# Optimization experiments

Hardware: AMD Instinct MI355X
Metric: run time of the kernel (lower is better)

Reference implementation:

```python
import jax, jax.numpy as jnp
from jax import lax
import numpy as np

D_MODEL = 1024
D_STATE = 16
D_CONV = 4
EXPAND = 2
D_INNER = EXPAND * D_MODEL
DT_RANK = -(-D_MODEL // D_STATE)  # ceil(d_model/d_state) = 64
BATCH, SEQ = 2, 2048


def setup_inputs() -> dict:
    key = jax.random.key(0)
    ks = jax.random.split(key, 12)
    s = lambda fan_in: 1.0 / np.sqrt(fan_in)
    inp = {
        "x": jax.random.normal(ks[0], (BATCH, SEQ, D_MODEL), jnp.float32),
        # weights stored as [in, out] (i.e. torch W.T) for y = x @ W + b
        "in_proj_w": jax.random.normal(ks[1], (D_MODEL, 2 * D_INNER), jnp.float32) * s(D_MODEL),
        "in_proj_b": jax.random.normal(ks[2], (2 * D_INNER,), jnp.float32) * s(D_MODEL),
        # depthwise conv weight in torch Conv1d layout [out_ch, in_ch/groups=1, k]
        "conv_w": jax.random.normal(ks[3], (D_INNER, 1, D_CONV), jnp.float32) * s(D_CONV),
        "conv_b": jax.random.normal(ks[4], (D_INNER,), jnp.float32) * s(D_CONV),
        "x_proj_w": jax.random.normal(ks[5], (D_INNER, DT_RANK + 2 * D_STATE), jnp.float32) * s(D_INNER),
        "dt_proj_w": jax.random.normal(ks[6], (DT_RANK, D_INNER), jnp.float32) * s(DT_RANK),
        "dt_proj_b": jax.random.normal(ks[7], (D_INNER,), jnp.float32) * s(DT_RANK),
        # log_A = log(arange(1, d_state+1)) repeated over d_inner rows
        "log_A": jnp.log(jnp.broadcast_to(jnp.arange(1, D_STATE + 1, dtype=jnp.float32), (D_INNER, D_STATE))),
        "D": jnp.ones((D_INNER,), jnp.float32),
        "out_proj_w": jax.random.normal(ks[8], (D_INNER, D_MODEL), jnp.float32) * s(D_INNER),
        "out_proj_b": jax.random.normal(ks[9], (D_MODEL,), jnp.float32) * s(D_INNER),
    }
    return inp


def reference(x, in_proj_w, in_proj_b, conv_w, conv_b, x_proj_w,
              dt_proj_w, dt_proj_b, log_A, D, out_proj_w, out_proj_b):
    batch, seq_len, _ = x.shape
    d_inner, d_state = log_A.shape
    d_conv = conv_w.shape[-1]
    dt_rank = dt_proj_w.shape[0]

    xr = x @ in_proj_w + in_proj_b                      # [B, L, 2*d_inner]
    x_val, res = jnp.split(xr, 2, axis=-1)

    # depthwise causal conv: torch pads both sides by d_conv-1 then keeps first L
    # outputs, which equals left-padding by d_conv-1.
    xv = x_val.transpose(0, 2, 1)                       # [B, C, L]
    xv = lax.conv_general_dilated(xv, conv_w, window_strides=(1,),
                                  padding=[(d_conv - 1, 0)],
                                  feature_group_count=d_inner)
    xv = xv + conv_b[None, :, None]
    x_val = jax.nn.silu(xv.transpose(0, 2, 1))          # [B, L, d_inner]

    x_dbl = x_val @ x_proj_w                            # [B, L, dt_rank + 2*d_state]
    dt = x_dbl[..., :dt_rank]
    Bm = x_dbl[..., dt_rank:dt_rank + d_state]          # [B, L, N]
    Cm = x_dbl[..., dt_rank + d_state:]                 # [B, L, N]
    dt = jax.nn.softplus(dt @ dt_proj_w + dt_proj_b)    # [B, L, d_inner]

    A = -jnp.exp(log_A)                                 # [d_inner, N]

    def step(h, inputs):
        dt_t, B_t, C_t, x_t = inputs                    # [B,d], [B,N], [B,N], [B,d]
        dA = jnp.exp(dt_t[:, :, None] * A)              # [B, d_inner, N]
        h = dA * h + (dt_t * x_t)[:, :, None] * B_t[:, None, :]
        y_t = jnp.einsum('bdn,bn->bd', h, C_t)
        return h, y_t

    h0 = jnp.zeros((batch, d_inner, d_state), x.dtype)
    xs = (dt.transpose(1, 0, 2), Bm.transpose(1, 0, 2),
          Cm.transpose(1, 0, 2), x_val.transpose(1, 0, 2))
    _, ys = lax.scan(step, h0, xs)                      # ys: [L, B, d_inner]

    y = ys.transpose(1, 0, 2) + x_val * D
    return (y * jax.nn.silu(res)) @ out_proj_w + out_proj_b
```

## Files before the change

### kernel.cpp

```cpp
#include <hip/hip_runtime.h>
#include <hip/hip_bf16.h>

#define BATCH 2
#define SEQ 2048
#define DM 1024
#define DI 2048
#define DS 16
#define DR 64
#define XPC 96
#define ROWS 4096
#define NC 32
#define CL 64
#define XRLD 4096
#define KSXP 8

typedef __attribute__((ext_vector_type(8))) short bf16x8;
typedef __attribute__((ext_vector_type(4))) float f32x4;
typedef unsigned short ushort_t;
typedef unsigned int u32;

#define GLD_LDS16(g, l) \
    __builtin_amdgcn_global_load_lds((const __attribute__((address_space(1))) u32*)(g), \
                                     (__attribute__((address_space(3))) u32*)(l), 16, 0, 0)

static __device__ __forceinline__ float bf2f(ushort_t u) {
    __hip_bfloat16 b = *(__hip_bfloat16*)&u;
    return __bfloat162float(b);
}
static __device__ __forceinline__ ushort_t f2bf(float f) {
    __hip_bfloat16 b = __float2bfloat16(f);
    return *(ushort_t*)&b;
}

__global__ __launch_bounds__(256) void cvt_f32_bf16(
    const float* __restrict__ in, ushort_t* __restrict__ out)
{
    const size_t i = (size_t)(blockIdx.x * 256 + threadIdx.x) * 4;
    float4 v = *(const float4*)(in + i);
    ushort4 o;
    o.x = f2bf(v.x); o.y = f2bf(v.y); o.z = f2bf(v.z); o.w = f2bf(v.w);
    *(ushort4*)(out + i) = o;
}

__global__ __launch_bounds__(256) void convt_bf16(
    const float* __restrict__ W, ushort_t* __restrict__ Wt, int K, int N)
{
    __shared__ float t[32][33];
    const int n0 = blockIdx.x * 32, k0 = blockIdx.y * 32;
    const int tx = threadIdx.x & 31, ty = threadIdx.x >> 5;
#pragma unroll
    for (int i = 0; i < 32; i += 8)
        t[ty + i][tx] = W[(size_t)(k0 + ty + i) * N + n0 + tx];
    __syncthreads();
#pragma unroll
    for (int i = 0; i < 32; i += 8)
        Wt[(size_t)(n0 + ty + i) * K + k0 + tx] = f2bf(t[tx][ty + i]);
}

template<int EPI, typename OutT>
__global__ __launch_bounds__(256) void gemm128_bt(
    const ushort_t* __restrict__ A, const ushort_t* __restrict__ Bt,
    const float* __restrict__ bias, OutT* __restrict__ C,
    int K, int ldc)
{
    __shared__ ushort_t As[2][128 * 32];
    __shared__ ushort_t Bs[2][128 * 32];
    const int tid = threadIdx.x;
    const int lane = tid & 63, wid = tid >> 6;
    const int quad = lane >> 4, l16 = lane & 15;
    const int wr = wid >> 1, wc = wid & 1;
    const int bm = blockIdx.y, bn = blockIdx.x;

    const int sr = tid >> 2, sk = (tid & 3) << 3;
    const ushort_t* Ag0 = A + (size_t)(bm * 128 + sr) * K + sk;
    const ushort_t* Ag1 = A + (size_t)(bm * 128 + 64 + sr) * K + sk;
    const ushort_t* Bg0 = Bt + (size_t)(bn * 128 + sr) * K + sk;
    const ushort_t* Bg1 = Bt + (size_t)(bn * 128 + 64 + sr) * K + sk;

    f32x4 acc[4][4];
#pragma unroll
    for (int m = 0; m < 4; ++m)
#pragma unroll
        for (int n = 0; n < 4; ++n) acc[m][n] = (f32x4){0.f, 0.f, 0.f, 0.f};

    auto stage = [&](int buf, int kk) {
        GLD_LDS16(Ag0 + kk, &As[buf][tid * 8]);
        GLD_LDS16(Ag1 + kk, &As[buf][(tid + 256) * 8]);
        GLD_LDS16(Bg0 + kk, &Bs[buf][tid * 8]);
        GLD_LDS16(Bg1 + kk, &Bs[buf][(tid + 256) * 8]);
    };
    auto compute = [&](int buf) {
        bf16x8 a[4], b[4];
#pragma unroll
        for (int m = 0; m < 4; ++m)
            a[m] = *(const bf16x8*)&As[buf][(wr * 64 + m * 16 + l16) * 32 + 8 * quad];
#pragma unroll
        for (int n = 0; n < 4; ++n)
            b[n] = *(const bf16x8*)&Bs[buf][(wc * 64 + n * 16 + l16) * 32 + 8 * quad];
#pragma unroll
        for (int m = 0; m < 4; ++m)
#pragma unroll
            for (int n = 0; n < 4; ++n)
                acc[m][n] = __builtin_amdgcn_mfma_f32_16x16x32_bf16(
                    a[m], b[n], acc[m][n], 0, 0, 0);
    };

    const int nt = K >> 5;
    stage(0, 0);
    for (int t = 0; t < nt; t += 2) {
        __syncthreads();
        if (t + 1 < nt) stage(1, (t + 1) << 5);
        compute(0);
        __syncthreads();
        if (t + 2 < nt) stage(0, (t + 2) << 5);
        compute(1);
    }

#pragma unroll
    for (int m = 0; m < 4; ++m) {
        const int row0 = bm * 128 + wr * 64 + m * 16 + quad * 4;
#pragma unroll
        for (int n = 0; n < 4; ++n) {
            const int col = bn * 128 + wc * 64 + n * 16 + l16;
            const float bv = bias ? bias[col] : 0.f;
#pragma unroll
            for (int r = 0; r < 4; ++r) {
                float v = acc[m][n][r] + bv;
                if constexpr (EPI == 1) {
                    ((ushort_t*)C)[(size_t)(row0 + r) * ldc + col] = f2bf(v);
                } else if constexpr (EPI == 2) {
                    float sp = (v > 20.f) ? v : log1pf(__expf(v));
                    ((float*)C)[(size_t)(row0 + r) * ldc + col] = sp;
                } else {
                    ((float*)C)[(size_t)(row0 + r) * ldc + col] = v;
                }
            }
        }
    }
}

__global__ __launch_bounds__(256) void xproj_splitk(
    const ushort_t* __restrict__ A, const ushort_t* __restrict__ Bt,
    float* __restrict__ part, int K)
{
    const int BM = 64, BN = XPC;
    __shared__ ushort_t As[64 * 40];
    __shared__ ushort_t Bs[XPC * 40];
    const int tid = threadIdx.x;
    const int wid = tid >> 6, lane = tid & 63;
    const int quad = lane >> 4, l16 = lane & 15;
    const int wr = wid;
    const int bm = blockIdx.y;
    const int ks = blockIdx.x;
    const int kslc = K / KSXP;
    const int kbeg = ks * kslc;

    f32x4 acc[6];
#pragma unroll
    for (int n = 0; n < 6; ++n) acc[n] = (f32x4){0.f, 0.f, 0.f, 0.f};

    for (int k0 = kbeg; k0 < kbeg + kslc; k0 += 32) {
        for (int i = tid; i < BM * 4; i += 256) {
            int r = i >> 2, kk = (i & 3) << 3;
            *(uint4*)&As[r * 40 + kk] =
                *(const uint4*)&A[(size_t)(bm * BM + r) * K + k0 + kk];
        }
        for (int i = tid; i < BN * 4; i += 256) {
            int r = i >> 2, kk = (i & 3) << 3;
            *(uint4*)&Bs[r * 40 + kk] =
                *(const uint4*)&Bt[(size_t)r * K + k0 + kk];
        }
        __syncthreads();
        bf16x8 a, b[6];
        a = *(const bf16x8*)&As[(wr * 16 + l16) * 40 + 8 * quad];
#pragma unroll
        for (int n = 0; n < 6; ++n)
            b[n] = *(const bf16x8*)&Bs[(n * 16 + l16) * 40 + 8 * quad];
#pragma unroll
        for (int n = 0; n < 6; ++n)
            acc[n] = __builtin_amdgcn_mfma_f32_16x16x32_bf16(a, b[n], acc[n], 0, 0, 0);
        __syncthreads();
    }

    float* out = part + (size_t)ks * ROWS * XPC;
    const int row0 = bm * BM + wr * 16 + quad * 4;
#pragma unroll
    for (int n = 0; n < 6; ++n) {
        const int col = n * 16 + l16;
#pragma unroll
        for (int r = 0; r < 4; ++r)
            out[(size_t)(row0 + r) * XPC + col] = acc[n][r];
    }
}

__global__ __launch_bounds__(256) void xproj_reduce(
    const float* __restrict__ part, float* __restrict__ xdbl,
    ushort_t* __restrict__ xdt)
{
    const size_t i = (size_t)(blockIdx.x * 256 + threadIdx.x) * 4;
    float4 s = *(const float4*)(part + i);
#pragma unroll
    for (int ks = 1; ks < KSXP; ++ks) {
        float4 v = *(const float4*)(part + (size_t)ks * ROWS * XPC + i);
        s.x += v.x; s.y += v.y; s.z += v.z; s.w += v.w;
    }
    *(float4*)(xdbl + i) = s;
    const int col = (int)(i % XPC);
    if (col < DR) {
        const int row = (int)(i / XPC);
        ushort4 o;
        o.x = f2bf(s.x); o.y = f2bf(s.y); o.z = f2bf(s.z); o.w = f2bf(s.w);
        *(ushort4*)(xdt + (size_t)row * DR + col) = o;
    }
}

__global__ __launch_bounds__(256) void conv_silu_kernel(
    const ushort_t* __restrict__ xr, const float* __restrict__ cw,
    const float* __restrict__ cb, ushort_t* __restrict__ xc)
{
    int idx = blockIdx.x * 256 + threadIdx.x;
    int r = idx >> 11;
    int d = idx & (DI - 1);
    int t = r & (SEQ - 1);
    float acc = cb[d];
#pragma unroll
    for (int k = 0; k < 4; ++k) {
        int tt = t - 3 + k;
        if (tt >= 0)
            acc += bf2f(xr[(size_t)(r - 3 + k) * XRLD + d]) * cw[d * 4 + k];
    }
    float sv = acc / (1.f + __expf(-acc));
    xc[idx] = f2bf(sv);
}


__global__ __launch_bounds__(256) void scan_pass1(
    const float* __restrict__ dt, const ushort_t* __restrict__ xc,
    const float* __restrict__ xdbl, const float* __restrict__ logA,
    float* __restrict__ hend, float* __restrict__ prodA)
{
    __shared__ float Bsm[CL][DS];
    const int bid = blockIdx.x;
    const int bc = bid >> 3;
    const int d = ((bid & 7) << 8) + threadIdx.x;
    const int c = bc & (NC - 1);
    const int b = bc >> 5;
    const int r0 = b * SEQ + c * CL;

    {
        int i = threadIdx.x;
        int r = i >> 2, n4 = (i & 3) << 2;
        *(float4*)&Bsm[r][n4] = *(const float4*)&xdbl[(size_t)(r0 + r) * XPC + DR + n4];
    }
    __syncthreads();

    float A[DS], h[DS];
#pragma unroll
    for (int n = 0; n < DS; ++n) {
        A[n] = -__expf(logA[d * DS + n]);
        h[n] = 0.f;
    }
    float dtsum = 0.f;
#pragma unroll 4
    for (int t = 0; t < CL; ++t) {
        const int r = r0 + t;
        float dtv = dt[(size_t)r * DI + d];
        float xv = bf2f(xc[(size_t)r * DI + d]);
        float bx = dtv * xv;
        dtsum += dtv;
#pragma unroll
        for (int n = 0; n < DS; ++n) {
            float dA = __expf(dtv * A[n]);
            h[n] = dA * h[n] + bx * Bsm[t][n];
        }
    }
#pragma unroll
    for (int n = 0; n < DS; ++n) {
        size_t o = ((size_t)bc * DS + n) * DI + d;
        hend[o] = h[n];
        prodA[o] = __expf(dtsum * A[n]);
    }
}

__global__ __launch_bounds__(256) void scan_pass2(
    const float* __restrict__ hend, const float* __restrict__ prodA,
    float* __restrict__ hin)
{
    const int gid = blockIdx.x * 256 + threadIdx.x;
    const int d = gid & (DI - 1);
    const int bn = gid >> 11;
    const int n = bn & (DS - 1);
    const int b = bn >> 4;
    float hprev = 0.f;
#pragma unroll 8
    for (int c = 0; c < NC; ++c) {
        size_t o = ((size_t)(b * NC + c) * DS + n) * DI + d;
        hin[o] = hprev;
        hprev = prodA[o] * hprev + hend[o];
    }
}

__global__ __launch_bounds__(256) void scan_pass3(
    const float* __restrict__ dt, const ushort_t* __restrict__ xc,
    const float* __restrict__ xdbl, const ushort_t* __restrict__ res,
    const float* __restrict__ logA, const float* __restrict__ Dp,
    const float* __restrict__ hin, ushort_t* __restrict__ yg)
{
    __shared__ float BCs[CL][2 * DS];
    const int bid = blockIdx.x;
    const int bc = bid >> 3;
    const int d = ((bid & 7) << 8) + threadIdx.x;
    const int c = bc & (NC - 1);
    const int b = bc >> 5;
    const int r0 = b * SEQ + c * CL;

    {
        int i = threadIdx.x;
        int r = i >> 3, c4 = (i & 7) << 2;
        *(float4*)&BCs[r][c4] = *(const float4*)&xdbl[(size_t)(r0 + r) * XPC + DR + c4];
        int i2 = i + 256;
        int r2 = i2 >> 3, c42 = (i2 & 7) << 2;
        *(float4*)&BCs[r2][c42] = *(const float4*)&xdbl[(size_t)(r0 + r2) * XPC + DR + c42];
    }
    __syncthreads();

    float A[DS], h[DS];
#pragma unroll
    for (int n = 0; n < DS; ++n) {
        A[n] = -__expf(logA[d * DS + n]);
        h[n] = hin[((size_t)bc * DS + n) * DI + d];
    }
    const float Dd = Dp[d];
#pragma unroll 4
    for (int t = 0; t < CL; ++t) {
        const int r = r0 + t;
        float dtv = dt[(size_t)r * DI + d];
        float xv = bf2f(xc[(size_t)r * DI + d]);
        float bx = dtv * xv;
        float y = 0.f;
#pragma unroll
        for (int n = 0; n < DS; ++n) {
            float dA = __expf(dtv * A[n]);
            h[n] = dA * h[n] + bx * BCs[t][n];
            y += h[n] * BCs[t][DS + n];
        }
        y += xv * Dd;
        float rv = bf2f(res[(size_t)r * XRLD + d]);
        float sr = rv / (1.f + __expf(-rv));
        yg[(size_t)r * DI + d] = f2bf(y * sr);
    }
}

extern "C" void kernel_launch(void* const* d_in, const int* in_sizes, int n_in,
                              void* d_out, int out_size, void* d_ws, size_t ws_size,
                              hipStream_t stream) {
    const float* x          = (const float*)d_in[0];
    const float* in_proj_w  = (const float*)d_in[1];
    const float* in_proj_b  = (const float*)d_in[2];
    const float* conv_w     = (const float*)d_in[3];
    const float* conv_b     = (const float*)d_in[4];
    const float* x_proj_w   = (const float*)d_in[5];
    const float* dt_proj_w  = (const float*)d_in[6];
    const float* dt_proj_b  = (const float*)d_in[7];
    const float* log_A      = (const float*)d_in[8];
    const float* Dp         = (const float*)d_in[9];
    const float* out_proj_w = (const float*)d_in[10];
    const float* out_proj_b = (const float*)d_in[11];

    float* ws    = (float*)d_ws;
    float* dt    = ws;
    float* part  = ws;
    float* xdbl  = dt    + (size_t)ROWS * DI;
    float* hend  = xdbl  + (size_t)ROWS * XPC;
    float* prodA = hend  + (size_t)BATCH * NC * DS * DI;
    float* hin   = prodA + (size_t)BATCH * NC * DS * DI;
    ushort_t* xr     = (ushort_t*)(hin + (size_t)BATCH * NC * DS * DI);
    ushort_t* xc_bf  = xr     + (size_t)ROWS * XRLD;
    ushort_t* yg_bf  = xc_bf  + (size_t)ROWS * DI;
    ushort_t* x_bf   = yg_bf  + (size_t)ROWS * DI;
    ushort_t* wt_in  = x_bf   + (size_t)ROWS * DM;
    ushort_t* wt_out = wt_in  + (size_t)2 * DI * DM;
    ushort_t* wt_xp  = wt_out + (size_t)DM * DI;
    ushort_t* wt_dt  = wt_xp  + (size_t)XPC * DI;
    ushort_t* xdt_bf = wt_dt  + (size_t)DI * DR;

    dim3 blk(256);

    cvt_f32_bf16<<<(ROWS * DM / 4) / 256, blk, 0, stream>>>(x, x_bf);
    convt_bf16<<<dim3(2 * DI / 32, DM / 32), blk, 0, stream>>>(in_proj_w, wt_in, DM, 2 * DI);
    convt_bf16<<<dim3(DM / 32, DI / 32), blk, 0, stream>>>(out_proj_w, wt_out, DI, DM);
    convt_bf16<<<dim3(XPC / 32, DI / 32), blk, 0, stream>>>(x_proj_w, wt_xp, DI, XPC);
    convt_bf16<<<dim3(DI / 32, DR / 32), blk, 0, stream>>>(dt_proj_w, wt_dt, DR, DI);

    gemm128_bt<1, ushort_t><<<dim3(XRLD / 128, ROWS / 128), blk, 0, stream>>>(
        x_bf, wt_in, in_proj_b, xr, DM, XRLD);

    conv_silu_kernel<<<(ROWS * DI) / 256, blk, 0, stream>>>(xr, conv_w, conv_b, xc_bf);

    xproj_splitk<<<dim3(KSXP, ROWS / 64), blk, 0, stream>>>(xc_bf, wt_xp, part, DI);
    xproj_reduce<<<(ROWS * XPC / 4) / 256, blk, 0, stream>>>(part, xdbl, xdt_bf);

    gemm128_bt<2, float><<<dim3(DI / 128, ROWS / 128), blk, 0, stream>>>(
        xdt_bf, wt_dt, dt_proj_b, dt, DR, DI);

    scan_pass1<<<BATCH * NC * (DI / 256), blk, 0, stream>>>(
        dt, xc_bf, xdbl, log_A, hend, prodA);
    scan_pass2<<<(BATCH * DS * DI) / 256, blk, 0, stream>>>(hend, prodA, hin);
    scan_pass3<<<BATCH * NC * (DI / 256), blk, 0, stream>>>(
        dt, xc_bf, xdbl, xr + DI, log_A, Dp, hin, yg_bf);

    gemm128_bt<0, float><<<dim3(DM / 128, ROWS / 128), blk, 0, stream>>>(
        yg_bf, wt_out, out_proj_b, (float*)d_out, DI, DM);
}
```

Measured before the change: 287.3 us.

## Merge weight transposes, vectorize conv, store dt in bf16, split-K out_proj

Folds the four weight-transpose launches into one kernel that dispatches on block index. The depthwise conv now handles four channels per thread with vector loads. The softplus dt output is stored as bf16 to halve dt traffic in both scan passes. The out-projection GEMM is split along K into two partial sums that a separate kernel adds together with the bias, which doubles the grid from 256 to 512 blocks at the cost of extra partial-sum traffic and reduced dt precision.

After: 277.5 us. 1.04x faster.

```diff
diff --git a/kernel.cpp b/kernel.cpp
--- a/kernel.cpp
+++ b/kernel.cpp
@@ -42,11 +42,20 @@
     *(ushort4*)(out + i) = o;
 }
 
-__global__ __launch_bounds__(256) void convt_bf16(
-    const float* __restrict__ W, ushort_t* __restrict__ Wt, int K, int N)
+__global__ __launch_bounds__(256) void convt_multi(
+    const float* __restrict__ ipw, ushort_t* __restrict__ wt_in,
+    const float* __restrict__ opw, ushort_t* __restrict__ wt_out,
+    const float* __restrict__ xpw, ushort_t* __restrict__ wt_xp,
+    const float* __restrict__ dpw, ushort_t* __restrict__ wt_dt)
 {
     __shared__ float t[32][33];
-    const int n0 = blockIdx.x * 32, k0 = blockIdx.y * 32;
+    int b = blockIdx.x;
+    const float* W; ushort_t* Wt; int K, N, nb;
+    if (b < 4096)      { W = ipw; Wt = wt_in;  K = 1024; N = 4096; nb = 128; }
+    else if (b < 6144) { b -= 4096; W = opw; Wt = wt_out; K = 2048; N = 1024; nb = 32; }
+    else if (b < 6336) { b -= 6144; W = xpw; Wt = wt_xp;  K = 2048; N = 96;   nb = 3;  }
+    else               { b -= 6336; W = dpw; Wt = wt_dt;  K = 64;   N = 2048; nb = 64; }
+    const int n0 = (b % nb) * 32, k0 = (b / nb) * 32;
     const int tx = threadIdx.x & 31, ty = threadIdx.x >> 5;
 #pragma unroll
     for (int i = 0; i < 32; i += 8)
@@ -57,7 +66,7 @@
         Wt[(size_t)(n0 + ty + i) * K + k0 + tx] = f2bf(t[tx][ty + i]);
 }
 
-template<int EPI, typename OutT>
+template<int EPI, typename OutT, int SPLITK>
 __global__ __launch_bounds__(256) void gemm128_bt(
     const ushort_t* __restrict__ A, const ushort_t* __restrict__ Bt,
     const float* __restrict__ bias, OutT* __restrict__ C,
@@ -69,13 +78,19 @@
     const int lane = tid & 63, wid = tid >> 6;
     const int quad = lane >> 4, l16 = lane & 15;
     const int wr = wid >> 1, wc = wid & 1;
-    const int bm = blockIdx.y, bn = blockIdx.x;
+    const int nbx = gridDim.x / SPLITK;
+    const int bn = blockIdx.x % nbx;
+    const int ks = blockIdx.x / nbx;
+    const int bm = blockIdx.y;
+    const int ksl = K / SPLITK;
+    const int kbeg = ks * ksl;
+    OutT* Cb = C + (size_t)ks * (size_t)gridDim.y * 128 * ldc;
 
     const int sr = tid >> 2, sk = (tid & 3) << 3;
-    const ushort_t* Ag0 = A + (size_t)(bm * 128 + sr) * K + sk;
-    const ushort_t* Ag1 = A + (size_t)(bm * 128 + 64 + sr) * K + sk;
-    const ushort_t* Bg0 = Bt + (size_t)(bn * 128 + sr) * K + sk;
-    const ushort_t* Bg1 = Bt + (size_t)(bn * 128 + 64 + sr) * K + sk;
+    const ushort_t* Ag0 = A + (size_t)(bm * 128 + sr) * K + kbeg + sk;
+    const ushort_t* Ag1 = A + (size_t)(bm * 128 + 64 + sr) * K + kbeg + sk;
+    const ushort_t* Bg0 = Bt + (size_t)(bn * 128 + sr) * K + kbeg + sk;
+    const ushort_t* Bg1 = Bt + (size_t)(bn * 128 + 64 + sr) * K + kbeg + sk;
 
     f32x4 acc[4][4];
 #pragma unroll
@@ -105,7 +120,7 @@
                     a[m], b[n], acc[m][n], 0, 0, 0);
     };
 
-    const int nt = K >> 5;
+    const int nt = ksl >> 5;
     stage(0, 0);
     for (int t = 0; t < nt; t += 2) {
         __syncthreads();
@@ -127,16 +142,33 @@
             for (int r = 0; r < 4; ++r) {
                 float v = acc[m][n][r] + bv;
                 if constexpr (EPI == 1) {
-                    ((ushort_t*)C)[(size_t)(row0 + r) * ldc + col] = f2bf(v);
+                    ((ushort_t*)Cb)[(size_t)(row0 + r) * ldc + col] = f2bf(v);
                 } else if constexpr (EPI == 2) {
                     float sp = (v > 20.f) ? v : log1pf(__expf(v));
-                    ((float*)C)[(size_t)(row0 + r) * ldc + col] = sp;
+                    ((float*)Cb)[(size_t)(row0 + r) * ldc + col] = sp;
+                } else if constexpr (EPI == 3) {
+                    float sp = (v > 20.f) ? v : log1pf(__expf(v));
+                    ((ushort_t*)Cb)[(size_t)(row0 + r) * ldc + col] = f2bf(sp);
                 } else {
-                    ((float*)C)[(size_t)(row0 + r) * ldc + col] = v;
+                    ((float*)Cb)[(size_t)(row0 + r) * ldc + col] = v;
                 }
             }
         }
     }
+}
+
+__global__ __launch_bounds__(256) void sum2_bias(
+    const float* __restrict__ part, const float* __restrict__ bias,
+    float* __restrict__ out)
+{
+    const size_t i = (size_t)(blockIdx.x * 256 + threadIdx.x) * 4;
+    float4 a = *(const float4*)(part + i);
+    float4 b = *(const float4*)(part + (size_t)ROWS * DM + i);
+    float4 bv = *(const float4*)(bias + (i & (DM - 1)));
+    float4 o;
+    o.x = a.x + b.x + bv.x; o.y = a.y + b.y + bv.y;
+    o.z = a.z + b.z + bv.z; o.w = a.w + b.w + bv.w;
+    *(float4*)(out + i) = o;
 }
 
 __global__ __launch_bounds__(256) void xproj_splitk(
@@ -218,24 +250,38 @@
     const ushort_t* __restrict__ xr, const float* __restrict__ cw,
     const float* __restrict__ cb, ushort_t* __restrict__ xc)
 {
-    int idx = blockIdx.x * 256 + threadIdx.x;
-    int r = idx >> 11;
-    int d = idx & (DI - 1);
-    int t = r & (SEQ - 1);
-    float acc = cb[d];
+    const int i = blockIdx.x * 256 + threadIdx.x;
+    const int r = i >> 9;
+    const int d0 = (i & 511) << 2;
+    const int t = r & (SEQ - 1);
+    float w[4][4];
+#pragma unroll
+    for (int j = 0; j < 4; ++j)
+        *(float4*)w[j] = *(const float4*)&cw[(d0 + j) * 4];
+    float4 bb = *(const float4*)&cb[d0];
+    float acc[4] = {bb.x, bb.y, bb.z, bb.w};
 #pragma unroll
     for (int k = 0; k < 4; ++k) {
         int tt = t - 3 + k;
-        if (tt >= 0)
-            acc += bf2f(xr[(size_t)(r - 3 + k) * XRLD + d]) * cw[d * 4 + k];
-    }
-    float sv = acc / (1.f + __expf(-acc));
-    xc[idx] = f2bf(sv);
+        if (tt >= 0) {
+            ushort4 v = *(const ushort4*)&xr[(size_t)(r - 3 + k) * XRLD + d0];
+            acc[0] += bf2f(v.x) * w[0][k];
+            acc[1] += bf2f(v.y) * w[1][k];
+            acc[2] += bf2f(v.z) * w[2][k];
+            acc[3] += bf2f(v.w) * w[3][k];
+        }
+    }
+    ushort4 o;
+    o.x = f2bf(acc[0] / (1.f + __expf(-acc[0])));
+    o.y = f2bf(acc[1] / (1.f + __expf(-acc[1])));
+    o.z = f2bf(acc[2] / (1.f + __expf(-acc[2])));
+    o.w = f2bf(acc[3] / (1.f + __expf(-acc[3])));
+    *(ushort4*)&xc[(size_t)r * DI + d0] = o;
 }
 
 
 __global__ __launch_bounds__(256) void scan_pass1(
-    const float* __restrict__ dt, const ushort_t* __restrict__ xc,
+    const ushort_t* __restrict__ dt, const ushort_t* __restrict__ xc,
     const float* __restrict__ xdbl, const float* __restrict__ logA,
     float* __restrict__ hend, float* __restrict__ prodA)
 {
@@ -264,7 +310,7 @@
 #pragma unroll 4
     for (int t = 0; t < CL; ++t) {
         const int r = r0 + t;
-        float dtv = dt[(size_t)r * DI + d];
+        float dtv = bf2f(dt[(size_t)r * DI + d]);
         float xv = bf2f(xc[(size_t)r * DI + d]);
         float bx = dtv * xv;
         dtsum += dtv;
@@ -301,7 +347,7 @@
 }
 
 __global__ __launch_bounds__(256) void scan_pass3(
-    const float* __restrict__ dt, const ushort_t* __restrict__ xc,
+    const ushort_t* __restrict__ dt, const ushort_t* __restrict__ xc,
     const float* __restrict__ xdbl, const ushort_t* __restrict__ res,
     const float* __restrict__ logA, const float* __restrict__ Dp,
     const float* __restrict__ hin, ushort_t* __restrict__ yg)
@@ -334,7 +380,7 @@
 #pragma unroll 4
     for (int t = 0; t < CL; ++t) {
         const int r = r0 + t;
-        float dtv = dt[(size_t)r * DI + d];
+        float dtv = bf2f(dt[(size_t)r * DI + d]);
         float xv = bf2f(xc[(size_t)r * DI + d]);
         float bx = dtv * xv;
         float y = 0.f;
@@ -368,12 +414,13 @@
     const float* out_proj_b = (const float*)d_in[11];
 
     float* ws    = (float*)d_ws;
-    float* dt    = ws;
-    float* part  = ws;
-    float* xdbl  = dt    + (size_t)ROWS * DI;
+    float*    part  = ws;
+    ushort_t* dt_bf = (ushort_t*)ws;
+    float* xdbl  = ws    + (size_t)ROWS * DI;
     float* hend  = xdbl  + (size_t)ROWS * XPC;
     float* prodA = hend  + (size_t)BATCH * NC * DS * DI;
     float* hin   = prodA + (size_t)BATCH * NC * DS * DI;
+    float* part_out = hend;
     ushort_t* xr     = (ushort_t*)(hin + (size_t)BATCH * NC * DS * DI);
     ushort_t* xc_bf  = xr     + (size_t)ROWS * XRLD;
     ushort_t* yg_bf  = xc_bf  + (size_t)ROWS * DI;
@@ -387,28 +434,28 @@
     dim3 blk(256);
 
     cvt_f32_bf16<<<(ROWS * DM / 4) / 256, blk, 0, stream>>>(x, x_bf);
-    convt_bf16<<<dim3(2 * DI / 32, DM / 32), blk, 0, stream>>>(in_proj_w, wt_in, DM, 2 * DI);
-    convt_bf16<<<dim3(DM / 32, DI / 32), blk, 0, stream>>>(out_proj_w, wt_out, DI, DM);
-    convt_bf16<<<dim3(XPC / 32, DI / 32), blk, 0, stream>>>(x_proj_w, wt_xp, DI, XPC);
-    convt_bf16<<<dim3(DI / 32, DR / 32), blk, 0, stream>>>(dt_proj_w, wt_dt, DR, DI);
-
-    gemm128_bt<1, ushort_t><<<dim3(XRLD / 128, ROWS / 128), blk, 0, stream>>>(
+    convt_multi<<<6464, blk, 0, stream>>>(in_proj_w, wt_in, out_proj_w, wt_out,
+                                          x_proj_w, wt_xp, dt_proj_w, wt_dt);
+
+    gemm128_bt<1, ushort_t, 1><<<dim3(XRLD / 128, ROWS / 128), blk, 0, stream>>>(
         x_bf, wt_in, in_proj_b, xr, DM, XRLD);
 
-    conv_silu_kernel<<<(ROWS * DI) / 256, blk, 0, stream>>>(xr, conv_w, conv_b, xc_bf);
+    conv_silu_kernel<<<(ROWS * DI / 4) / 256, blk, 0, stream>>>(xr, conv_w, conv_b, xc_bf);
 
     xproj_splitk<<<dim3(KSXP, ROWS / 64), blk, 0, stream>>>(xc_bf, wt_xp, part, DI);
     xproj_reduce<<<(ROWS * XPC / 4) / 256, blk, 0, stream>>>(part, xdbl, xdt_bf);
 
-    gemm128_bt<2, float><<<dim3(DI / 128, ROWS / 128), blk, 0, stream>>>(
-        xdt_bf, wt_dt, dt_proj_b, dt, DR, DI);
+    gemm128_bt<3, ushort_t, 1><<<dim3(DI / 128, ROWS / 128), blk, 0, stream>>>(
+        xdt_bf, wt_dt, dt_proj_b, dt_bf, DR, DI);
 
     scan_pass1<<<BATCH * NC * (DI / 256), blk, 0, stream>>>(
-        dt, xc_bf, xdbl, log_A, hend, prodA);
+        dt_bf, xc_bf, xdbl, log_A, hend, prodA);
     scan_pass2<<<(BATCH * DS * DI) / 256, blk, 0, stream>>>(hend, prodA, hin);
     scan_pass3<<<BATCH * NC * (DI / 256), blk, 0, stream>>>(
-        dt, xc_bf, xdbl, xr + DI, log_A, Dp, hin, yg_bf);
-
-    gemm128_bt<0, float><<<dim3(DM / 128, ROWS / 128), blk, 0, stream>>>(
-        yg_bf, wt_out, out_proj_b, (float*)d_out, DI, DM);
-}
+        dt_bf, xc_bf, xdbl, xr + DI, log_A, Dp, hin, yg_bf);
+
+    gemm128_bt<0, float, 2><<<dim3(2 * DM / 128, ROWS / 128), blk, 0, stream>>>(
+        yg_bf, wt_out, nullptr, part_out, DI, DM);
+    sum2_bias<<<(ROWS * DM / 4) / 256, blk, 0, stream>>>(
+        part_out, out_proj_b, (float*)d_out);
+}
```
